# Kernel optimization log

Hardware: AMD Instinct MI355X
Metric: run time of the kernel (lower is better)

Reference implementation:

```python
import jax, jax.numpy as jnp
import numpy as np

H = 64
NG = 100000   # gene nodes
ND = 30000    # disease nodes
NE = 1500000  # gda edges (gene -> disease)
NL = 500000   # supervision (label) edges


def setup_inputs() -> dict:
    key = jax.random.key(0)
    ks = jax.random.split(key, 20)
    s = 0.1
    inp = {
        "gene_emb":    jax.random.normal(ks[0], (NG, H), jnp.float32) * s,
        "disease_emb": jax.random.normal(ks[1], (ND, H), jnp.float32) * s,
    }
    wnames = ["w1_gd_l", "w1_gd_r", "w1_dg_l", "w1_dg_r",
              "w2_gd_l", "w2_gd_r", "w2_dg_l", "w2_dg_r"]
    for i, n in enumerate(wnames):
        inp[n] = jax.random.normal(ks[2 + i], (H, H), jnp.float32) * s
    for i, n in enumerate(["b1_gd", "b1_dg", "b2_gd", "b2_dg"]):
        inp[n] = jax.random.normal(ks[10 + i], (H,), jnp.float32) * 0.01
    inp["edge_src"]  = jax.random.randint(ks[14], (NE,), 0, NG)
    inp["edge_dst"]  = jax.random.randint(ks[15], (NE,), 0, ND)
    inp["label_src"] = jax.random.randint(ks[16], (NL,), 0, NG)
    inp["label_dst"] = jax.random.randint(ks[17], (NL,), 0, ND)
    return inp


def _sage(x_src, x_dst, src, dst, n_dst, wl, wr, b):
    # SAGEConv (mean aggr): lin_l(mean_{j in N(i)} x_j) + lin_r(x_i) + b
    msum = jax.ops.segment_sum(x_src[src], dst, num_segments=n_dst)
    cnt = jax.ops.segment_sum(jnp.ones((src.shape[0], 1), x_src.dtype), dst,
                              num_segments=n_dst)
    mean = msum / jnp.maximum(cnt, 1.0)
    return mean @ wl + x_dst @ wr + b


def reference(gene_emb, disease_emb,
              w1_gd_l, w1_gd_r, b1_gd, w1_dg_l, w1_dg_r, b1_dg,
              w2_gd_l, w2_gd_r, b2_gd, w2_dg_l, w2_dg_r, b2_dg,
              edge_src, edge_dst, label_src, label_dst):
    # layer 1 (hetero: gene->disease via gda, disease->gene via rev_gda)
    h_d = jax.nn.relu(_sage(gene_emb, disease_emb, edge_src, edge_dst, ND,
                            w1_gd_l, w1_gd_r, b1_gd))
    h_g = jax.nn.relu(_sage(disease_emb, gene_emb, edge_dst, edge_src, NG,
                            w1_dg_l, w1_dg_r, b1_dg))
    # layer 2 (no activation)
    h_d2 = _sage(h_g, h_d, edge_src, edge_dst, ND, w2_gd_l, w2_gd_r, b2_gd)
    h_g2 = _sage(h_d, h_g, edge_dst, edge_src, NG, w2_dg_l, w2_dg_r, b2_dg)
    # classifier: dot product over label edges
    return jnp.sum(h_g2[label_src] * h_d2[label_dst], axis=-1)
```

## Files before the change

### kernel.cpp

```cpp
#include <hip/hip_runtime.h>
#include <hip/hip_bf16.h>

#define H 64
#define SCAN_CHUNK 512
#define NB1 512

typedef unsigned short u16;
typedef unsigned int u32;
typedef unsigned char u8;
typedef __attribute__((ext_vector_type(8))) __bf16 bf16x8;
typedef __attribute__((ext_vector_type(4))) float f32x4;
typedef __attribute__((ext_vector_type(2))) float f32x2;

__device__ __forceinline__ float bflo(u32 u) {
    return __builtin_bit_cast(float, u << 16);
}
__device__ __forceinline__ float bfhi(u32 u) {
    return __builtin_bit_cast(float, u & 0xffff0000u);
}
__device__ __forceinline__ u16 bf16rne(float f) {
    u32 u = __builtin_bit_cast(u32, f);
    return (u16)((u + 0x7FFFu + ((u >> 16) & 1u)) >> 16);
}

__global__ __launch_bounds__(256) void fused_count_convert_kernel(
    const int* __restrict__ es, const int* __restrict__ ed,
    int* __restrict__ histD, int* __restrict__ histG,
    int ne, int shiftD, int shiftG,
    const float* __restrict__ a, u16* __restrict__ oa, u32* __restrict__ oa8,
    long long na4,
    const float* __restrict__ b, u16* __restrict__ ob, long long nb4)
{
    if (blockIdx.x < NB1) {
        __shared__ int lhd[256], lhg[256];
        const int tid = threadIdx.x;
        lhd[tid] = 0; lhg[tid] = 0;
        __syncthreads();
        const int chunk = (ne + NB1 - 1) / NB1;
        const int e0 = blockIdx.x * chunk;
        const int e1 = min(e0 + chunk, ne);
        for (int e = e0 + tid; e < e1; e += 256) {
            atomicAdd(&lhd[ed[e] >> shiftD], 1);
            atomicAdd(&lhg[es[e] >> shiftG], 1);
        }
        __syncthreads();
        histD[tid * NB1 + blockIdx.x] = lhd[tid];
        histG[tid * NB1 + blockIdx.x] = lhg[tid];
        return;
    }
    long long i = (long long)(blockIdx.x - NB1) * 256 + threadIdx.x;
    if (i < na4) {
        float4 v = *(const float4*)&a[i * 4];
        ushort4 o;
        o.x = bf16rne(v.x); o.y = bf16rne(v.y);
        o.z = bf16rne(v.z); o.w = bf16rne(v.w);
        *(ushort4*)&oa[i * 4] = o;
        int r = 0;
        r = __builtin_amdgcn_cvt_pk_fp8_f32(v.x * 16.0f, v.y * 16.0f, r, false);
        r = __builtin_amdgcn_cvt_pk_fp8_f32(v.z * 16.0f, v.w * 16.0f, r, true);
        oa8[i] = (u32)r;
    } else if (i < na4 + nb4) {
        long long q = i - na4;
        float4 v = *(const float4*)&b[q * 4];
        ushort4 o;
        o.x = bf16rne(v.x); o.y = bf16rne(v.y);
        o.z = bf16rne(v.z); o.w = bf16rne(v.w);
        *(ushort4*)&ob[q * 4] = o;
    }
}

__global__ __launch_bounds__(256) void scan_reduce_kernel(
    const int* __restrict__ a1, int n1, const int* __restrict__ a2, int n2,
    int B1, int* __restrict__ partial)
{
    const int b = blockIdx.x;
    const int* a; int n, base;
    if (b < B1) { a = a1; n = n1; base = b * SCAN_CHUNK; }
    else        { a = a2; n = n2; base = (b - B1) * SCAN_CHUNK; }
    int t = threadIdx.x;
    int i0 = base + 2 * t, i1 = i0 + 1;
    int v = ((i0 < n) ? a[i0] : 0) + ((i1 < n) ? a[i1] : 0);
    #pragma unroll
    for (int off = 32; off > 0; off >>= 1) v += __shfl_down(v, off, 64);
    __shared__ int ws[4];
    if ((t & 63) == 0) ws[t >> 6] = v;
    __syncthreads();
    if (t == 0) partial[b] = ws[0] + ws[1] + ws[2] + ws[3];
}

__global__ __launch_bounds__(256) void scan_apply_kernel(
    const int* __restrict__ a1, int* __restrict__ out1, int n1,
    const int* __restrict__ a2, int* __restrict__ out2, int n2,
    int B1, int nbtot, const int* __restrict__ partial)
{
    __shared__ int sExcl[1024];
    __shared__ int ws[4];
    const int tid = threadIdx.x;
    const int lane = tid & 63, wid = tid >> 6;

    int j0 = 4 * tid;
    int p0 = (j0 + 0 < nbtot) ? partial[j0 + 0] : 0;
    int p1 = (j0 + 1 < nbtot) ? partial[j0 + 1] : 0;
    int p2 = (j0 + 2 < nbtot) ? partial[j0 + 2] : 0;
    int p3 = (j0 + 3 < nbtot) ? partial[j0 + 3] : 0;
    int psum = p0 + p1 + p2 + p3;
    int P = psum;
    #pragma unroll
    for (int off = 1; off < 64; off <<= 1) {
        int u = __shfl_up(P, off, 64);
        if (lane >= off) P += u;
    }
    if (lane == 63) ws[wid] = P;
    __syncthreads();
    int wbase = 0;
    #pragma unroll
    for (int w = 0; w < 4; ++w) wbase += (w < wid) ? ws[w] : 0;
    int e = wbase + (P - psum);
    sExcl[j0 + 0] = e;
    sExcl[j0 + 1] = e + p0;
    sExcl[j0 + 2] = e + p0 + p1;
    sExcl[j0 + 3] = e + p0 + p1 + p2;
    __syncthreads();

    const int b = blockIdx.x;
    int tot1 = sExcl[B1 - 1] + partial[B1 - 1];
    int myOff = sExcl[b] - ((b >= B1) ? tot1 : 0);
    if (b == 0 && tid == 0) {
        int tot2 = sExcl[nbtot - 1] + partial[nbtot - 1] - tot1;
        out1[n1] = tot1;
        out2[n2] = tot2;
    }
    __syncthreads();

    const int* a; int* out; int n, base;
    if (b < B1) { a = a1; out = out1; n = n1; base = b * SCAN_CHUNK; }
    else        { a = a2; out = out2; n = n2; base = (b - B1) * SCAN_CHUNK; }
    int i0 = base + 2 * tid, i1 = i0 + 1;
    int x0 = (i0 < n) ? a[i0] : 0;
    int x1 = (i1 < n) ? a[i1] : 0;
    int p = x0 + x1;
    int Q = p;
    #pragma unroll
    for (int off = 1; off < 64; off <<= 1) {
        int u = __shfl_up(Q, off, 64);
        if (lane >= off) Q += u;
    }
    if (lane == 63) ws[wid] = Q;
    __syncthreads();
    int waveBase = 0;
    #pragma unroll
    for (int w = 0; w < 4; ++w) waveBase += (w < wid) ? ws[w] : 0;
    int off0 = myOff + waveBase + (Q - p);
    if (i0 < n) out[i0] = off0;
    if (i1 < n) out[i1] = off0 + x0;
}

__global__ __launch_bounds__(256) void part_scatter_kernel(
    const int* __restrict__ es, const int* __restrict__ ed,
    const int* __restrict__ baseD, const int* __restrict__ baseG,
    u32* __restrict__ pairD, u32* __restrict__ pairG,
    int ne, int shiftD, int shiftG)
{
    __shared__ int curD[256], curG[256];
    const int tid = threadIdx.x;
    curD[tid] = baseD[tid * NB1 + blockIdx.x];
    curG[tid] = baseG[tid * NB1 + blockIdx.x];
    __syncthreads();
    const int maskD = (1 << shiftD) - 1;
    const int maskG = (1 << shiftG) - 1;
    const int chunk = (ne + NB1 - 1) / NB1;
    const int e0 = blockIdx.x * chunk;
    const int e1 = min(e0 + chunk, ne);
    for (int e = e0 + tid; e < e1; e += 256) {
        int s = es[e], d = ed[e];
        int pD = atomicAdd(&curD[d >> shiftD], 1);
        pairD[pD] = ((u32)(d & maskD) << 17) | (u32)s;
        int pG = atomicAdd(&curG[s >> shiftG], 1);
        pairG[pG] = ((u32)(s & maskG) << 17) | (u32)d;
    }
}

__global__ __launch_bounds__(256) void csr_build_kernel(
    const u32* __restrict__ pairD, const int* __restrict__ baseD,
    int* __restrict__ rowD, int* __restrict__ idxD, int nd, int shiftD, int nbktD,
    const u32* __restrict__ pairG, const int* __restrict__ baseG,
    int* __restrict__ rowG, int* __restrict__ idxG, int ng, int shiftG, int nbktG)
{
    __shared__ int lcnt[512], lcur[512];
    __shared__ int ws[4];
    const int j = blockIdx.x & 255;
    const int isG = blockIdx.x >> 8;
    const u32* pair; const int* base; int* row; int* idx; int n, shift, nbkt;
    if (isG) { pair = pairG; base = baseG; row = rowG; idx = idxG; n = ng; shift = shiftG; nbkt = nbktG; }
    else     { pair = pairD; base = baseD; row = rowD; idx = idxD; n = nd; shift = shiftD; nbkt = nbktD; }
    if (j >= nbkt) return;

    const int tid = threadIdx.x;
    const int nLo = j << shift;
    const int nHi = min(nLo + (1 << shift), n);
    const int range = nHi - nLo;
    const int segBase = base[j * NB1];
    const int segEnd  = base[(j + 1) * NB1];

    lcnt[tid] = 0; lcnt[tid + 256] = 0;
    __syncthreads();
    for (int t = segBase + tid; t < segEnd; t += 256)
        atomicAdd(&lcnt[pair[t] >> 17], 1);
    __syncthreads();

    int i0 = 2 * tid, i1 = i0 + 1;
    int c0 = (i0 < range) ? lcnt[i0] : 0;
    int c1 = (i1 < range) ? lcnt[i1] : 0;
    int p = c0 + c1;
    int P = p;
    const int lane = tid & 63, wid = tid >> 6;
    #pragma unroll
    for (int off = 1; off < 64; off <<= 1) {
        int u = __shfl_up(P, off, 64);
        if (lane >= off) P += u;
    }
    if (lane == 63) ws[wid] = P;
    __syncthreads();
    int waveBase = 0;
    #pragma unroll
    for (int w = 0; w < 4; ++w) waveBase += (w < wid) ? ws[w] : 0;
    int o0 = segBase + waveBase + (P - p);
    int o1 = o0 + c0;
    if (i0 < range) { row[nLo + i0] = o0; lcur[i0] = o0; }
    if (i1 < range) { row[nLo + i1] = o1; lcur[i1] = o1; }
    if (nHi == n && tid == 0) row[n] = segEnd;
    __syncthreads();

    for (int t = segBase + tid; t < segEnd; t += 256) {
        u32 pr = pair[t];
        int pos = atomicAdd(&lcur[pr >> 17], 1);
        idx[pos] = (int)(pr & 0x1FFFFu);
    }
}

template <bool F8D>
__global__ __launch_bounds__(256) void gather_mean_kernel(
    const void* __restrict__ srcD_, const u16* __restrict__ srcG,
    const int* __restrict__ rowD, const int* __restrict__ idxD,
    const int* __restrict__ rowG, const int* __restrict__ idxG,
    u16* __restrict__ outD, u16* __restrict__ outG, int nd, int ng)
{
    int hw = blockIdx.x * 8 + (threadIdx.x >> 5);
    int l5 = threadIdx.x & 31;
    if (hw >= nd + ng) return;
    const bool isD = hw < nd;
    const int sub = l5 >> 3;
    const int c8 = l5 & 7;
    const int* row; const int* idx; u16* out; int node;
    if (isD) { row = rowD; idx = idxD; out = outD; node = hw; }
    else     { row = rowG; idx = idxG; out = outG; node = hw - nd; }
    int beg = row[node], end = row[node + 1];

    float a0[8], a1[8];
    #pragma unroll
    for (int j = 0; j < 8; ++j) { a0[j] = 0.f; a1[j] = 0.f; }

    if (F8D && isD) {
        const u8* src8 = (const u8*)srcD_;
        int i = beg;
        for (; i + 8 <= end; i += 8) {
            int s0 = idx[i + sub];
            int s1 = idx[i + 4 + sub];
            uint2 v0 = *((const uint2*)(src8 + (size_t)s0 * 64) + c8);
            uint2 v1 = *((const uint2*)(src8 + (size_t)s1 * 64) + c8);
            f32x2 f;
            f = __builtin_amdgcn_cvt_pk_f32_fp8((int)v0.x, false); a0[0] += f.x; a0[1] += f.y;
            f = __builtin_amdgcn_cvt_pk_f32_fp8((int)v0.x, true);  a0[2] += f.x; a0[3] += f.y;
            f = __builtin_amdgcn_cvt_pk_f32_fp8((int)v0.y, false); a0[4] += f.x; a0[5] += f.y;
            f = __builtin_amdgcn_cvt_pk_f32_fp8((int)v0.y, true);  a0[6] += f.x; a0[7] += f.y;
            f = __builtin_amdgcn_cvt_pk_f32_fp8((int)v1.x, false); a1[0] += f.x; a1[1] += f.y;
            f = __builtin_amdgcn_cvt_pk_f32_fp8((int)v1.x, true);  a1[2] += f.x; a1[3] += f.y;
            f = __builtin_amdgcn_cvt_pk_f32_fp8((int)v1.y, false); a1[4] += f.x; a1[5] += f.y;
            f = __builtin_amdgcn_cvt_pk_f32_fp8((int)v1.y, true);  a1[6] += f.x; a1[7] += f.y;
        }
        if (i + 4 <= end) {
            int s0 = idx[i + sub];
            uint2 v0 = *((const uint2*)(src8 + (size_t)s0 * 64) + c8);
            f32x2 f;
            f = __builtin_amdgcn_cvt_pk_f32_fp8((int)v0.x, false); a0[0] += f.x; a0[1] += f.y;
            f = __builtin_amdgcn_cvt_pk_f32_fp8((int)v0.x, true);  a0[2] += f.x; a0[3] += f.y;
            f = __builtin_amdgcn_cvt_pk_f32_fp8((int)v0.y, false); a0[4] += f.x; a0[5] += f.y;
            f = __builtin_amdgcn_cvt_pk_f32_fp8((int)v0.y, true);  a0[6] += f.x; a0[7] += f.y;
            i += 4;
        }
        if (i + sub < end) {
            int s1 = idx[i + sub];
            uint2 v1 = *((const uint2*)(src8 + (size_t)s1 * 64) + c8);
            f32x2 f;
            f = __builtin_amdgcn_cvt_pk_f32_fp8((int)v1.x, false); a1[0] += f.x; a1[1] += f.y;
            f = __builtin_amdgcn_cvt_pk_f32_fp8((int)v1.x, true);  a1[2] += f.x; a1[3] += f.y;
            f = __builtin_amdgcn_cvt_pk_f32_fp8((int)v1.y, false); a1[4] += f.x; a1[5] += f.y;
            f = __builtin_amdgcn_cvt_pk_f32_fp8((int)v1.y, true);  a1[6] += f.x; a1[7] += f.y;
        }
    } else {
        const u16* src = isD ? (const u16*)srcD_ : srcG;
        int i = beg;
        for (; i + 8 <= end; i += 8) {
            int s0 = idx[i + sub];
            int s1 = idx[i + 4 + sub];
            uint4 v0 = *((const uint4*)(src + (size_t)s0 * H) + c8);
            uint4 v1 = *((const uint4*)(src + (size_t)s1 * H) + c8);
            a0[0] += bflo(v0.x); a0[1] += bfhi(v0.x); a0[2] += bflo(v0.y); a0[3] += bfhi(v0.y);
            a0[4] += bflo(v0.z); a0[5] += bfhi(v0.z); a0[6] += bflo(v0.w); a0[7] += bfhi(v0.w);
            a1[0] += bflo(v1.x); a1[1] += bfhi(v1.x); a1[2] += bflo(v1.y); a1[3] += bfhi(v1.y);
            a1[4] += bflo(v1.z); a1[5] += bfhi(v1.z); a1[6] += bflo(v1.w); a1[7] += bfhi(v1.w);
        }
        if (i + 4 <= end) {
            int s0 = idx[i + sub];
            uint4 v0 = *((const uint4*)(src + (size_t)s0 * H) + c8);
            a0[0] += bflo(v0.x); a0[1] += bfhi(v0.x); a0[2] += bflo(v0.y); a0[3] += bfhi(v0.y);
            a0[4] += bflo(v0.z); a0[5] += bfhi(v0.z); a0[6] += bflo(v0.w); a0[7] += bfhi(v0.w);
            i += 4;
        }
        if (i + sub < end) {
            int s1 = idx[i + sub];
            uint4 v1 = *((const uint4*)(src + (size_t)s1 * H) + c8);
            a1[0] += bflo(v1.x); a1[1] += bfhi(v1.x); a1[2] += bflo(v1.y); a1[3] += bfhi(v1.y);
            a1[4] += bflo(v1.z); a1[5] += bfhi(v1.z); a1[6] += bflo(v1.w); a1[7] += bfhi(v1.w);
        }
    }

    float acc[8];
    #pragma unroll
    for (int j = 0; j < 8; ++j) acc[j] = a0[j] + a1[j];
    #pragma unroll
    for (int j = 0; j < 8; ++j) {
        acc[j] += __shfl_xor(acc[j], 8, 64);
        acc[j] += __shfl_xor(acc[j], 16, 64);
    }
    if (sub == 0) {
        float inv = 1.0f / fmaxf((float)(end - beg), 1.0f);
        if (F8D && isD) inv *= 0.0625f;
        u32 w0 = (u32)bf16rne(acc[0] * inv) | ((u32)bf16rne(acc[1] * inv) << 16);
        u32 w1 = (u32)bf16rne(acc[2] * inv) | ((u32)bf16rne(acc[3] * inv) << 16);
        u32 w2 = (u32)bf16rne(acc[4] * inv) | ((u32)bf16rne(acc[5] * inv) << 16);
        u32 w3 = (u32)bf16rne(acc[6] * inv) | ((u32)bf16rne(acc[7] * inv) << 16);
        uint4 pk = make_uint4(w0, w1, w2, w3);
        *(uint4*)(out + (size_t)node * H + c8 * 8) = pk;
    }
}

template <bool RELU>
__global__ __launch_bounds__(256) void sage_mm_mfma_kernel(
    const u16* __restrict__ meanD, const u16* __restrict__ xD, u16* __restrict__ outD,
    const float* __restrict__ wlD, const float* __restrict__ wrD,
    const float* __restrict__ bD, int nd,
    const u16* __restrict__ meanG, const u16* __restrict__ xG, u16* __restrict__ outG,
    const float* __restrict__ wlG, const float* __restrict__ wrG,
    const float* __restrict__ bG, int ng, int MBD)
{
    __shared__ u16 sB[16 * 64 * 8];
    int b = blockIdx.x;
    const u16 *mean, *x; u16* out; const float *wl, *wr, *bias; int n;
    if (b < MBD) { mean = meanD; x = xD; out = outD; wl = wlD; wr = wrD; bias = bD; n = nd; }
    else { b -= MBD; mean = meanG; x = xG; out = outG; wl = wlG; wr = wrG; bias = bG; n = ng; }

    const int tid = threadIdx.x;
    for (int i = tid; i < 4096; i += 256) {
        int k = i >> 6, ncol = i & 63;
        int q = (k >> 3) & 3, j = k & 7, t = ncol >> 4, n15 = ncol & 15;
        int lane = q * 16 + n15;
        int c0 = k >> 5;
        sB[(((c0 + 0) * 4 + t) * 64 + lane) * 8 + j] = bf16rne(wl[i]);
        sB[(((c0 + 2) * 4 + t) * 64 + lane) * 8 + j] = bf16rne(wr[i]);
    }
    __syncthreads();

    const int lane = tid & 63;
    const int wave = tid >> 6;
    const int m = lane & 15;
    const int q = lane >> 4;

    bf16x8 Bf[16];
    {
        const uint4* sB4 = (const uint4*)sB;
        #pragma unroll
        for (int f = 0; f < 16; ++f)
            Bf[f] = __builtin_bit_cast(bf16x8, sB4[f * 64 + lane]);
    }
    float bv[4];
    #pragma unroll
    for (int t = 0; t < 4; ++t) bv[t] = bias[t * 16 + m];

    const int row0 = b * 256;
    #pragma unroll
    for (int r = 0; r < 4; ++r) {
        int rbase = row0 + (wave + 4 * r) * 16;
        if (rbase >= n) break;
        int gr = min(rbase + m, n - 1);
        const uint4* mrow = (const uint4*)(mean + (size_t)gr * H);
        const uint4* xrow = (const uint4*)(x + (size_t)gr * H);
        bf16x8 A0 = __builtin_bit_cast(bf16x8, mrow[q]);
        bf16x8 A1 = __builtin_bit_cast(bf16x8, mrow[q + 4]);
        bf16x8 A2 = __builtin_bit_cast(bf16x8, xrow[q]);
        bf16x8 A3 = __builtin_bit_cast(bf16x8, xrow[q + 4]);
        f32x4 acc[4];
        #pragma unroll
        for (int t = 0; t < 4; ++t) acc[t] = (f32x4){bv[t], bv[t], bv[t], bv[t]};
        #pragma unroll
        for (int t = 0; t < 4; ++t) {
            acc[t] = __builtin_amdgcn_mfma_f32_16x16x32_bf16(A0, Bf[0 * 4 + t], acc[t], 0, 0, 0);
            acc[t] = __builtin_amdgcn_mfma_f32_16x16x32_bf16(A1, Bf[1 * 4 + t], acc[t], 0, 0, 0);
            acc[t] = __builtin_amdgcn_mfma_f32_16x16x32_bf16(A2, Bf[2 * 4 + t], acc[t], 0, 0, 0);
            acc[t] = __builtin_amdgcn_mfma_f32_16x16x32_bf16(A3, Bf[3 * 4 + t], acc[t], 0, 0, 0);
        }
        #pragma unroll
        for (int reg = 0; reg < 4; ++reg) {
            int orow = rbase + q * 4 + reg;
            if (orow < n) {
                u16* op = out + (size_t)orow * H;
                #pragma unroll
                for (int t = 0; t < 4; ++t) {
                    float v = acc[t][reg];
                    if (RELU) v = fmaxf(v, 0.0f);
                    op[t * 16 + m] = bf16rne(v);
                }
            }
        }
    }
}

__global__ __launch_bounds__(256) void classify_kernel(
    const u16* __restrict__ hg2, const u16* __restrict__ hd2,
    const int* __restrict__ ls, const int* __restrict__ ld,
    float* __restrict__ out, int nl)
{
    long long t = (long long)blockIdx.x * blockDim.x + threadIdx.x;
    int e = (int)(t >> 3);
    int c8 = (int)(t & 7);
    if (e >= nl) return;
    int a = ls[e];
    int b = ld[e];
    uint4 ua = *((const uint4*)(hg2 + (size_t)a * H) + c8);
    uint4 ub = *((const uint4*)(hd2 + (size_t)b * H) + c8);
    float v = bflo(ua.x) * bflo(ub.x) + bfhi(ua.x) * bfhi(ub.x)
            + bflo(ua.y) * bflo(ub.y) + bfhi(ua.y) * bfhi(ub.y)
            + bflo(ua.z) * bflo(ub.z) + bfhi(ua.z) * bfhi(ub.z)
            + bflo(ua.w) * bflo(ub.w) + bfhi(ua.w) * bfhi(ub.w);
    v += __shfl_xor(v, 1, 64);
    v += __shfl_xor(v, 2, 64);
    v += __shfl_xor(v, 4, 64);
    if (c8 == 0) out[e] = v;
}

extern "C" void kernel_launch(void* const* d_in, const int* in_sizes, int n_in,
                              void* d_out, int out_size, void* d_ws, size_t ws_size,
                              hipStream_t stream)
{
    const float* gene  = (const float*)d_in[0];
    const float* dis   = (const float*)d_in[1];
    const float* w1gdl = (const float*)d_in[2];
    const float* w1gdr = (const float*)d_in[3];
    const float* w1dgl = (const float*)d_in[4];
    const float* w1dgr = (const float*)d_in[5];
    const float* w2gdl = (const float*)d_in[6];
    const float* w2gdr = (const float*)d_in[7];
    const float* w2dgl = (const float*)d_in[8];
    const float* w2dgr = (const float*)d_in[9];
    const float* b1gd  = (const float*)d_in[10];
    const float* b1dg  = (const float*)d_in[11];
    const float* b2gd  = (const float*)d_in[12];
    const float* b2dg  = (const float*)d_in[13];
    const int* es = (const int*)d_in[14];
    const int* ed = (const int*)d_in[15];
    const int* ls = (const int*)d_in[16];
    const int* ld = (const int*)d_in[17];

    const int ng = in_sizes[0] / H;
    const int nd = in_sizes[1] / H;
    const int ne = in_sizes[14];
    const int nl = in_sizes[16];

    int shiftD = 0; while (((nd + (1 << shiftD) - 1) >> shiftD) > 256) ++shiftD;
    int shiftG = 0; while (((ng + (1 << shiftG) - 1) >> shiftG) > 256) ++shiftG;
    const int nbktD = (nd + (1 << shiftD) - 1) >> shiftD;
    const int nbktG = (ng + (1 << shiftG) - 1) >> shiftG;
    const int n1 = 256 * NB1;

    int* rowD = (int*)d_ws;
    int* rowG = rowD + nd + 1;
    int* idxD = rowG + ng + 1;
    int* idxG = idxD + ne;
    u16* geneBf = (u16*)(idxG + ne);
    u16* disBf  = geneBf + (size_t)ng * H;
    u16* h1Dbf  = disBf + (size_t)nd * H;
    u16* h1Gbf  = h1Dbf + (size_t)nd * H;
    u16* h2Dbf  = h1Gbf + (size_t)ng * H;
    u16* h2Gbf  = h2Dbf + (size_t)nd * H;
    uintptr_t pf8 = (uintptr_t)(h2Gbf + (size_t)ng * H);
    pf8 = (pf8 + 15) & ~(uintptr_t)15;
    u32* geneF8 = (u32*)pf8;
    uintptr_t p = (uintptr_t)(geneF8 + (size_t)ng * 16);
    p = (p + 15) & ~(uintptr_t)15;
    u16* MD = (u16*)p;
    u16* MG = MD + (size_t)nd * H;
    int* histD = (int*)p;
    int* histG = histD + n1;
    int* baseD = histG + n1;
    int* baseG = baseD + n1 + 1;
    int* partial  = baseG + n1 + 1;
    uintptr_t pp = (uintptr_t)(partial + 1024);
    pp = (pp + 15) & ~(uintptr_t)15;
    u32* pairD = (u32*)pp;
    u32* pairG = pairD + ne;

    const long long na4 = (long long)ng * H / 4;
    const long long nb4 = (long long)nd * H / 4;
    const int convBlocks = (int)((na4 + nb4 + 255) / 256);
    fused_count_convert_kernel<<<NB1 + convBlocks, 256, 0, stream>>>(
        es, ed, histD, histG, ne, shiftD, shiftG,
        gene, geneBf, geneF8, na4, dis, disBf, nb4);

    const int B1 = n1 / SCAN_CHUNK;
    const int nbtot = 2 * B1;
    scan_reduce_kernel<<<nbtot, 256, 0, stream>>>(histD, n1, histG, n1, B1, partial);
    scan_apply_kernel<<<nbtot, 256, 0, stream>>>(histD, baseD, n1,
                                                 histG, baseG, n1, B1, nbtot, partial);

    part_scatter_kernel<<<NB1, 256, 0, stream>>>(es, ed, baseD, baseG,
                                                 pairD, pairG, ne, shiftD, shiftG);
    csr_build_kernel<<<512, 256, 0, stream>>>(
        pairD, baseD, rowD, idxD, nd, shiftD, nbktD,
        pairG, baseG, rowG, idxG, ng, shiftG, nbktG);

    const int gatherBlocks = (nd + ng + 7) / 8;
    const int MBD = (nd + 255) / 256;
    const int MBG = (ng + 255) / 256;

    gather_mean_kernel<true><<<gatherBlocks, 256, 0, stream>>>(
        geneF8, disBf, rowD, idxD, rowG, idxG, MD, MG, nd, ng);
    sage_mm_mfma_kernel<true><<<MBD + MBG, 256, 0, stream>>>(
        MD, disBf, h1Dbf, w1gdl, w1gdr, b1gd, nd,
        MG, geneBf, h1Gbf, w1dgl, w1dgr, b1dg, ng, MBD);

    gather_mean_kernel<false><<<gatherBlocks, 256, 0, stream>>>(
        h1Gbf, h1Dbf, rowD, idxD, rowG, idxG, MD, MG, nd, ng);
    sage_mm_mfma_kernel<false><<<MBD + MBG, 256, 0, stream>>>(
        MD, h1Dbf, h2Dbf, w2gdl, w2gdr, b2gd, nd,
        MG, h1Gbf, h2Gbf, w2dgl, w2dgr, b2dg, ng, MBD);

    {
        long long threads = (long long)nl * 8;
        int blocks = (int)((threads + 255) / 256);
        classify_kernel<<<blocks, 256, 0, stream>>>(h2Gbf, h2Dbf, ls, ld,
                                                    (float*)d_out, nl);
    }
}
```

Measured before the change: 349.8 us.

## Fuse neighbor mean gather into MFMA SAGE matmul and bucket-sort label edges

Merges the gather-mean kernel and the MFMA linear kernel into one 512-thread kernel. Each block gathers 128 rows of neighbor means into shared memory and then multiplies them, so the mean buffers no longer make a round trip through global memory and two launches per layer are dropped. It also adds a bucket partition of label edges by source gene, reusing the histogram, scan and scatter stages, so the classifier reads gene rows in near-sorted order for better cache locality. The cost is more shared memory per block, heavier per-block work, and extra preprocessing passes over the label edges.

```diff
diff --git a/kernel.cpp b/kernel.cpp
--- a/kernel.cpp
+++ b/kernel.cpp
@@ -4,6 +4,9 @@
 #define H 64
 #define SCAN_CHUNK 512
 #define NB1 512
+#define NBL 256
+#define MROWS 128
+#define MSTRIDE 72
 
 typedef unsigned short u16;
 typedef unsigned int u32;
@@ -27,6 +30,7 @@
     const int* __restrict__ es, const int* __restrict__ ed,
     int* __restrict__ histD, int* __restrict__ histG,
     int ne, int shiftD, int shiftG,
+    const int* __restrict__ ls, int* __restrict__ histL, int nl,
     const float* __restrict__ a, u16* __restrict__ oa, u32* __restrict__ oa8,
     long long na4,
     const float* __restrict__ b, u16* __restrict__ ob, long long nb4)
@@ -48,7 +52,22 @@
         histG[tid * NB1 + blockIdx.x] = lhg[tid];
         return;
     }
-    long long i = (long long)(blockIdx.x - NB1) * 256 + threadIdx.x;
+    if (blockIdx.x < NB1 + NBL) {
+        __shared__ int lhl[256];
+        const int tid = threadIdx.x;
+        const int blk = blockIdx.x - NB1;
+        lhl[tid] = 0;
+        __syncthreads();
+        const int chunk = (nl + NBL - 1) / NBL;
+        const int e0 = blk * chunk;
+        const int e1 = min(e0 + chunk, nl);
+        for (int e = e0 + tid; e < e1; e += 256)
+            atomicAdd(&lhl[ls[e] >> shiftG], 1);
+        __syncthreads();
+        histL[tid * NBL + blk] = lhl[tid];
+        return;
+    }
+    long long i = (long long)(blockIdx.x - NB1 - NBL) * 256 + threadIdx.x;
     if (i < na4) {
         float4 v = *(const float4*)&a[i * 4];
         ushort4 o;
@@ -70,13 +89,15 @@
 }
 
 __global__ __launch_bounds__(256) void scan_reduce_kernel(
-    const int* __restrict__ a1, int n1, const int* __restrict__ a2, int n2,
-    int B1, int* __restrict__ partial)
+    const int* __restrict__ a1, int n1_, const int* __restrict__ a2, int n2_,
+    const int* __restrict__ a3, int n3_, int B1, int B2,
+    int* __restrict__ partial)
 {
     const int b = blockIdx.x;
     const int* a; int n, base;
-    if (b < B1) { a = a1; n = n1; base = b * SCAN_CHUNK; }
-    else        { a = a2; n = n2; base = (b - B1) * SCAN_CHUNK; }
+    if (b < B1)          { a = a1; n = n1_; base = b * SCAN_CHUNK; }
+    else if (b < B1 + B2){ a = a2; n = n2_; base = (b - B1) * SCAN_CHUNK; }
+    else                 { a = a3; n = n3_; base = (b - B1 - B2) * SCAN_CHUNK; }
     int t = threadIdx.x;
     int i0 = base + 2 * t, i1 = i0 + 1;
     int v = ((i0 < n) ? a[i0] : 0) + ((i1 < n) ? a[i1] : 0);
@@ -89,9 +110,10 @@
 }
 
 __global__ __launch_bounds__(256) void scan_apply_kernel(
-    const int* __restrict__ a1, int* __restrict__ out1, int n1,
-    const int* __restrict__ a2, int* __restrict__ out2, int n2,
-    int B1, int nbtot, const int* __restrict__ partial)
+    const int* __restrict__ a1, int* __restrict__ out1, int n1_,
+    const int* __restrict__ a2, int* __restrict__ out2, int n2_,
+    const int* __restrict__ a3, int* __restrict__ out3, int n3_,
+    int B1, int B2, int nbtot, const int* __restrict__ partial)
 {
     __shared__ int sExcl[1024];
     __shared__ int ws[4];
@@ -124,17 +146,21 @@
 
     const int b = blockIdx.x;
     int tot1 = sExcl[B1 - 1] + partial[B1 - 1];
-    int myOff = sExcl[b] - ((b >= B1) ? tot1 : 0);
+    int totA = sExcl[B1 + B2 - 1] + partial[B1 + B2 - 1];
+    int tot2 = totA - tot1;
+    int myOff = sExcl[b] - ((b >= B1) ? tot1 : 0) - ((b >= B1 + B2) ? tot2 : 0);
     if (b == 0 && tid == 0) {
-        int tot2 = sExcl[nbtot - 1] + partial[nbtot - 1] - tot1;
-        out1[n1] = tot1;
-        out2[n2] = tot2;
+        int tot3 = sExcl[nbtot - 1] + partial[nbtot - 1] - totA;
+        out1[n1_] = tot1;
+        out2[n2_] = tot2;
+        out3[n3_] = tot3;
     }
     __syncthreads();
 
     const int* a; int* out; int n, base;
-    if (b < B1) { a = a1; out = out1; n = n1; base = b * SCAN_CHUNK; }
-    else        { a = a2; out = out2; n = n2; base = (b - B1) * SCAN_CHUNK; }
+    if (b < B1)          { a = a1; out = out1; n = n1_; base = b * SCAN_CHUNK; }
+    else if (b < B1 + B2){ a = a2; out = out2; n = n2_; base = (b - B1) * SCAN_CHUNK; }
+    else                 { a = a3; out = out3; n = n3_; base = (b - B1 - B2) * SCAN_CHUNK; }
     int i0 = base + 2 * tid, i1 = i0 + 1;
     int x0 = (i0 < n) ? a[i0] : 0;
     int x1 = (i1 < n) ? a[i1] : 0;
@@ -159,24 +185,39 @@
     const int* __restrict__ es, const int* __restrict__ ed,
     const int* __restrict__ baseD, const int* __restrict__ baseG,
     u32* __restrict__ pairD, u32* __restrict__ pairG,
-    int ne, int shiftD, int shiftG)
-{
-    __shared__ int curD[256], curG[256];
+    int ne, int shiftD, int shiftG,
+    const int* __restrict__ ls, const int* __restrict__ baseL,
+    int* __restrict__ permL, int nl)
+{
+    __shared__ int curA[256], curB[256];
     const int tid = threadIdx.x;
-    curD[tid] = baseD[tid * NB1 + blockIdx.x];
-    curG[tid] = baseG[tid * NB1 + blockIdx.x];
-    __syncthreads();
-    const int maskD = (1 << shiftD) - 1;
-    const int maskG = (1 << shiftG) - 1;
-    const int chunk = (ne + NB1 - 1) / NB1;
-    const int e0 = blockIdx.x * chunk;
-    const int e1 = min(e0 + chunk, ne);
-    for (int e = e0 + tid; e < e1; e += 256) {
-        int s = es[e], d = ed[e];
-        int pD = atomicAdd(&curD[d >> shiftD], 1);
-        pairD[pD] = ((u32)(d & maskD) << 17) | (u32)s;
-        int pG = atomicAdd(&curG[s >> shiftG], 1);
-        pairG[pG] = ((u32)(s & maskG) << 17) | (u32)d;
+    if (blockIdx.x < NB1) {
+        curA[tid] = baseD[tid * NB1 + blockIdx.x];
+        curB[tid] = baseG[tid * NB1 + blockIdx.x];
+        __syncthreads();
+        const int maskD = (1 << shiftD) - 1;
+        const int maskG = (1 << shiftG) - 1;
+        const int chunk = (ne + NB1 - 1) / NB1;
+        const int e0 = blockIdx.x * chunk;
+        const int e1 = min(e0 + chunk, ne);
+        for (int e = e0 + tid; e < e1; e += 256) {
+            int s = es[e], d = ed[e];
+            int pD = atomicAdd(&curA[d >> shiftD], 1);
+            pairD[pD] = ((u32)(d & maskD) << 17) | (u32)s;
+            int pG = atomicAdd(&curB[s >> shiftG], 1);
+            pairG[pG] = ((u32)(s & maskG) << 17) | (u32)d;
+        }
+    } else {
+        const int blk = blockIdx.x - NB1;
+        curA[tid] = baseL[tid * NBL + blk];
+        __syncthreads();
+        const int chunk = (nl + NBL - 1) / NBL;
+        const int e0 = blk * chunk;
+        const int e1 = min(e0 + chunk, nl);
+        for (int e = e0 + tid; e < e1; e += 256) {
+            int pos = atomicAdd(&curA[ls[e] >> shiftG], 1);
+            permL[pos] = e;
+        }
     }
 }
 
@@ -238,130 +279,37 @@
     }
 }
 
-template <bool F8D>
-__global__ __launch_bounds__(256) void gather_mean_kernel(
-    const void* __restrict__ srcD_, const u16* __restrict__ srcG,
+template <bool RELU, bool F8D>
+__global__ __launch_bounds__(512, 8) void fused_gather_mm_kernel(
+    const void* __restrict__ gsrcD, const u16* __restrict__ gsrcG,
     const int* __restrict__ rowD, const int* __restrict__ idxD,
     const int* __restrict__ rowG, const int* __restrict__ idxG,
-    u16* __restrict__ outD, u16* __restrict__ outG, int nd, int ng)
-{
-    int hw = blockIdx.x * 8 + (threadIdx.x >> 5);
-    int l5 = threadIdx.x & 31;
-    if (hw >= nd + ng) return;
-    const bool isD = hw < nd;
-    const int sub = l5 >> 3;
-    const int c8 = l5 & 7;
-    const int* row; const int* idx; u16* out; int node;
-    if (isD) { row = rowD; idx = idxD; out = outD; node = hw; }
-    else     { row = rowG; idx = idxG; out = outG; node = hw - nd; }
-    int beg = row[node], end = row[node + 1];
-
-    float a0[8], a1[8];
-    #pragma unroll
-    for (int j = 0; j < 8; ++j) { a0[j] = 0.f; a1[j] = 0.f; }
-
-    if (F8D && isD) {
-        const u8* src8 = (const u8*)srcD_;
-        int i = beg;
-        for (; i + 8 <= end; i += 8) {
-            int s0 = idx[i + sub];
-            int s1 = idx[i + 4 + sub];
-            uint2 v0 = *((const uint2*)(src8 + (size_t)s0 * 64) + c8);
-            uint2 v1 = *((const uint2*)(src8 + (size_t)s1 * 64) + c8);
-            f32x2 f;
-            f = __builtin_amdgcn_cvt_pk_f32_fp8((int)v0.x, false); a0[0] += f.x; a0[1] += f.y;
-            f = __builtin_amdgcn_cvt_pk_f32_fp8((int)v0.x, true);  a0[2] += f.x; a0[3] += f.y;
-            f = __builtin_amdgcn_cvt_pk_f32_fp8((int)v0.y, false); a0[4] += f.x; a0[5] += f.y;
-            f = __builtin_amdgcn_cvt_pk_f32_fp8((int)v0.y, true);  a0[6] += f.x; a0[7] += f.y;
-            f = __builtin_amdgcn_cvt_pk_f32_fp8((int)v1.x, false); a1[0] += f.x; a1[1] += f.y;
-            f = __builtin_amdgcn_cvt_pk_f32_fp8((int)v1.x, true);  a1[2] += f.x; a1[3] += f.y;
-            f = __builtin_amdgcn_cvt_pk_f32_fp8((int)v1.y, false); a1[4] += f.x; a1[5] += f.y;
-            f = __builtin_amdgcn_cvt_pk_f32_fp8((int)v1.y, true);  a1[6] += f.x; a1[7] += f.y;
-        }
-        if (i + 4 <= end) {
-            int s0 = idx[i + sub];
-            uint2 v0 = *((const uint2*)(src8 + (size_t)s0 * 64) + c8);
-            f32x2 f;
-            f = __builtin_amdgcn_cvt_pk_f32_fp8((int)v0.x, false); a0[0] += f.x; a0[1] += f.y;
-            f = __builtin_amdgcn_cvt_pk_f32_fp8((int)v0.x, true);  a0[2] += f.x; a0[3] += f.y;
-            f = __builtin_amdgcn_cvt_pk_f32_fp8((int)v0.y, false); a0[4] += f.x; a0[5] += f.y;
-            f = __builtin_amdgcn_cvt_pk_f32_fp8((int)v0.y, true);  a0[6] += f.x; a0[7] += f.y;
-            i += 4;
-        }
-        if (i + sub < end) {
-            int s1 = idx[i + sub];
-            uint2 v1 = *((const uint2*)(src8 + (size_t)s1 * 64) + c8);
-            f32x2 f;
-            f = __builtin_amdgcn_cvt_pk_f32_fp8((int)v1.x, false); a1[0] += f.x; a1[1] += f.y;
-            f = __builtin_amdgcn_cvt_pk_f32_fp8((int)v1.x, true);  a1[2] += f.x; a1[3] += f.y;
-            f = __builtin_amdgcn_cvt_pk_f32_fp8((int)v1.y, false); a1[4] += f.x; a1[5] += f.y;
-            f = __builtin_amdgcn_cvt_pk_f32_fp8((int)v1.y, true);  a1[6] += f.x; a1[7] += f.y;
-        }
+    const u16* __restrict__ xD, const u16* __restrict__ xG,
+    u16* __restrict__ outD, u16* __restrict__ outG,
+    const float* __restrict__ wlD, const float* __restrict__ wrD,
+    const float* __restrict__ bD,
+    const float* __restrict__ wlG, const float* __restrict__ wrG,
+    const float* __restrict__ bG,
+    int nd, int ng, int MBD)
+{
+    __shared__ u16 sB[16 * 64 * 8];
+    __shared__ u16 sM[MROWS * MSTRIDE];
+
+    int b = blockIdx.x;
+    const void* gsrc; const int* row; const int* idx; const u16* x; u16* out;
+    const float *wl, *wr, *bias; int n; bool isD;
+    if (b < MBD) {
+        isD = true;  gsrc = gsrcD; row = rowD; idx = idxD; x = xD; out = outD;
+        wl = wlD; wr = wrD; bias = bD; n = nd;
     } else {
-        const u16* src = isD ? (const u16*)srcD_ : srcG;
-        int i = beg;
-        for (; i + 8 <= end; i += 8) {
-            int s0 = idx[i + sub];
-            int s1 = idx[i + 4 + sub];
-            uint4 v0 = *((const uint4*)(src + (size_t)s0 * H) + c8);
-            uint4 v1 = *((const uint4*)(src + (size_t)s1 * H) + c8);
-            a0[0] += bflo(v0.x); a0[1] += bfhi(v0.x); a0[2] += bflo(v0.y); a0[3] += bfhi(v0.y);
-            a0[4] += bflo(v0.z); a0[5] += bfhi(v0.z); a0[6] += bflo(v0.w); a0[7] += bfhi(v0.w);
-            a1[0] += bflo(v1.x); a1[1] += bfhi(v1.x); a1[2] += bflo(v1.y); a1[3] += bfhi(v1.y);
-            a1[4] += bflo(v1.z); a1[5] += bfhi(v1.z); a1[6] += bflo(v1.w); a1[7] += bfhi(v1.w);
-        }
-        if (i + 4 <= end) {
-            int s0 = idx[i + sub];
-            uint4 v0 = *((const uint4*)(src + (size_t)s0 * H) + c8);
-            a0[0] += bflo(v0.x); a0[1] += bfhi(v0.x); a0[2] += bflo(v0.y); a0[3] += bfhi(v0.y);
-            a0[4] += bflo(v0.z); a0[5] += bfhi(v0.z); a0[6] += bflo(v0.w); a0[7] += bfhi(v0.w);
-            i += 4;
-        }
-        if (i + sub < end) {
-            int s1 = idx[i + sub];
-            uint4 v1 = *((const uint4*)(src + (size_t)s1 * H) + c8);
-            a1[0] += bflo(v1.x); a1[1] += bfhi(v1.x); a1[2] += bflo(v1.y); a1[3] += bfhi(v1.y);
-            a1[4] += bflo(v1.z); a1[5] += bfhi(v1.z); a1[6] += bflo(v1.w); a1[7] += bfhi(v1.w);
-        }
-    }
-
-    float acc[8];
-    #pragma unroll
-    for (int j = 0; j < 8; ++j) acc[j] = a0[j] + a1[j];
-    #pragma unroll
-    for (int j = 0; j < 8; ++j) {
-        acc[j] += __shfl_xor(acc[j], 8, 64);
-        acc[j] += __shfl_xor(acc[j], 16, 64);
-    }
-    if (sub == 0) {
-        float inv = 1.0f / fmaxf((float)(end - beg), 1.0f);
-        if (F8D && isD) inv *= 0.0625f;
-        u32 w0 = (u32)bf16rne(acc[0] * inv) | ((u32)bf16rne(acc[1] * inv) << 16);
-        u32 w1 = (u32)bf16rne(acc[2] * inv) | ((u32)bf16rne(acc[3] * inv) << 16);
-        u32 w2 = (u32)bf16rne(acc[4] * inv) | ((u32)bf16rne(acc[5] * inv) << 16);
-        u32 w3 = (u32)bf16rne(acc[6] * inv) | ((u32)bf16rne(acc[7] * inv) << 16);
-        uint4 pk = make_uint4(w0, w1, w2, w3);
-        *(uint4*)(out + (size_t)node * H + c8 * 8) = pk;
-    }
-}
-
-template <bool RELU>
-__global__ __launch_bounds__(256) void sage_mm_mfma_kernel(
-    const u16* __restrict__ meanD, const u16* __restrict__ xD, u16* __restrict__ outD,
-    const float* __restrict__ wlD, const float* __restrict__ wrD,
-    const float* __restrict__ bD, int nd,
-    const u16* __restrict__ meanG, const u16* __restrict__ xG, u16* __restrict__ outG,
-    const float* __restrict__ wlG, const float* __restrict__ wrG,
-    const float* __restrict__ bG, int ng, int MBD)
-{
-    __shared__ u16 sB[16 * 64 * 8];
-    int b = blockIdx.x;
-    const u16 *mean, *x; u16* out; const float *wl, *wr, *bias; int n;
-    if (b < MBD) { mean = meanD; x = xD; out = outD; wl = wlD; wr = wrD; bias = bD; n = nd; }
-    else { b -= MBD; mean = meanG; x = xG; out = outG; wl = wlG; wr = wrG; bias = bG; n = ng; }
-
+        b -= MBD;
+        isD = false; gsrc = (const void*)gsrcG; row = rowG; idx = idxG; x = xG;
+        out = outG; wl = wlG; wr = wrG; bias = bG; n = ng;
+    }
+    const int row0 = b * MROWS;
     const int tid = threadIdx.x;
-    for (int i = tid; i < 4096; i += 256) {
+
+    for (int i = tid; i < 4096; i += 512) {
         int k = i >> 6, ncol = i & 63;
         int q = (k >> 3) & 3, j = k & 7, t = ncol >> 4, n15 = ncol & 15;
         int lane = q * 16 + n15;
@@ -369,57 +317,150 @@
         sB[(((c0 + 0) * 4 + t) * 64 + lane) * 8 + j] = bf16rne(wl[i]);
         sB[(((c0 + 2) * 4 + t) * 64 + lane) * 8 + j] = bf16rne(wr[i]);
     }
+
+    {
+        const int hw = tid >> 5;
+        const int l5 = tid & 31;
+        const int sub = l5 >> 3;
+        const int c8 = l5 & 7;
+        for (int t = 0; t < 8; ++t) {
+            int lr = hw * 8 + t;
+            int node = row0 + lr;
+            if (node >= n) break;
+            int beg = row[node], end = row[node + 1];
+            float a0[8], a1[8];
+            #pragma unroll
+            for (int j = 0; j < 8; ++j) { a0[j] = 0.f; a1[j] = 0.f; }
+
+            if (F8D && isD) {
+                const u8* src8 = (const u8*)gsrc;
+                int i = beg;
+                for (; i + 8 <= end; i += 8) {
+                    int s0 = idx[i + sub];
+                    int s1 = idx[i + 4 + sub];
+                    uint2 v0 = *((const uint2*)(src8 + (size_t)s0 * 64) + c8);
+                    uint2 v1 = *((const uint2*)(src8 + (size_t)s1 * 64) + c8);
+                    f32x2 f;
+                    f = __builtin_amdgcn_cvt_pk_f32_fp8((int)v0.x, false); a0[0] += f.x; a0[1] += f.y;
+                    f = __builtin_amdgcn_cvt_pk_f32_fp8((int)v0.x, true);  a0[2] += f.x; a0[3] += f.y;
+                    f = __builtin_amdgcn_cvt_pk_f32_fp8((int)v0.y, false); a0[4] += f.x; a0[5] += f.y;
+                    f = __builtin_amdgcn_cvt_pk_f32_fp8((int)v0.y, true);  a0[6] += f.x; a0[7] += f.y;
+                    f = __builtin_amdgcn_cvt_pk_f32_fp8((int)v1.x, false); a1[0] += f.x; a1[1] += f.y;
+                    f = __builtin_amdgcn_cvt_pk_f32_fp8((int)v1.x, true);  a1[2] += f.x; a1[3] += f.y;
+                    f = __builtin_amdgcn_cvt_pk_f32_fp8((int)v1.y, false); a1[4] += f.x; a1[5] += f.y;
+                    f = __builtin_amdgcn_cvt_pk_f32_fp8((int)v1.y, true);  a1[6] += f.x; a1[7] += f.y;
+                }
+                if (i + 4 <= end) {
+                    int s0 = idx[i + sub];
+                    uint2 v0 = *((const uint2*)(src8 + (size_t)s0 * 64) + c8);
+                    f32x2 f;
+                    f = __builtin_amdgcn_cvt_pk_f32_fp8((int)v0.x, false); a0[0] += f.x; a0[1] += f.y;
+                    f = __builtin_amdgcn_cvt_pk_f32_fp8((int)v0.x, true);  a0[2] += f.x; a0[3] += f.y;
+                    f = __builtin_amdgcn_cvt_pk_f32_fp8((int)v0.y, false); a0[4] += f.x; a0[5] += f.y;
+                    f = __builtin_amdgcn_cvt_pk_f32_fp8((int)v0.y, true);  a0[6] += f.x; a0[7] += f.y;
+                    i += 4;
+                }
+                if (i + sub < end) {
+                    int s1 = idx[i + sub];
+                    uint2 v1 = *((const uint2*)(src8 + (size_t)s1 * 64) + c8);
+                    f32x2 f;
+                    f = __builtin_amdgcn_cvt_pk_f32_fp8((int)v1.x, false); a1[0] += f.x; a1[1] += f.y;
+                    f = __builtin_amdgcn_cvt_pk_f32_fp8((int)v1.x, true);  a1[2] += f.x; a1[3] += f.y;
+                    f = __builtin_amdgcn_cvt_pk_f32_fp8((int)v1.y, false); a1[4] += f.x; a1[5] += f.y;
+                    f = __builtin_amdgcn_cvt_pk_f32_fp8((int)v1.y, true);  a1[6] += f.x; a1[7] += f.y;
+                }
+            } else {
+                const u16* src = (const u16*)gsrc;
+                int i = beg;
+                for (; i + 8 <= end; i += 8) {
+                    int s0 = idx[i + sub];
+                    int s1 = idx[i + 4 + sub];
+                    uint4 v0 = *((const uint4*)(src + (size_t)s0 * H) + c8);
+                    uint4 v1 = *((const uint4*)(src + (size_t)s1 * H) + c8);
+                    a0[0] += bflo(v0.x); a0[1] += bfhi(v0.x); a0[2] += bflo(v0.y); a0[3] += bfhi(v0.y);
+                    a0[4] += bflo(v0.z); a0[5] += bfhi(v0.z); a0[6] += bflo(v0.w); a0[7] += bfhi(v0.w);
+                    a1[0] += bflo(v1.x); a1[1] += bfhi(v1.x); a1[2] += bflo(v1.y); a1[3] += bfhi(v1.y);
+                    a1[4] += bflo(v1.z); a1[5] += bfhi(v1.z); a1[6] += bflo(v1.w); a1[7] += bfhi(v1.w);
+                }
+                if (i + 4 <= end) {
+                    int s0 = idx[i + sub];
+                    uint4 v0 = *((const uint4*)(src + (size_t)s0 * H) + c8);
+                    a0[0] += bflo(v0.x); a0[1] += bfhi(v0.x); a0[2] += bflo(v0.y); a0[3] += bfhi(v0.y);
+                    a0[4] += bflo(v0.z); a0[5] += bfhi(v0.z); a0[6] += bflo(v0.w); a0[7] += bfhi(v0.w);
+                    i += 4;
+                }
+                if (i + sub < end) {
+                    int s1 = idx[i + sub];
+                    uint4 v1 = *((const uint4*)(src + (size_t)s1 * H) + c8);
+                    a1[0] += bflo(v1.x); a1[1] += bfhi(v1.x); a1[2] += bflo(v1.y); a1[3] += bfhi(v1.y);
+                    a1[4] += bflo(v1.z); a1[5] += bfhi(v1.z); a1[6] += bflo(v1.w); a1[7] += bfhi(v1.w);
+                }
+            }
+
+            float acc[8];
+            #pragma unroll
+            for (int j = 0; j < 8; ++j) acc[j] = a0[j] + a1[j];
+            #pragma unroll
+            for (int j = 0; j < 8; ++j) {
+                acc[j] += __shfl_xor(acc[j], 8, 64);
+                acc[j] += __shfl_xor(acc[j], 16, 64);
+            }
+            if (sub == 0) {
+                float inv = 1.0f / fmaxf((float)(end - beg), 1.0f);
+                if (F8D && isD) inv *= 0.0625f;
+                u32 w0 = (u32)bf16rne(acc[0] * inv) | ((u32)bf16rne(acc[1] * inv) << 16);
+                u32 w1 = (u32)bf16rne(acc[2] * inv) | ((u32)bf16rne(acc[3] * inv) << 16);
+                u32 w2 = (u32)bf16rne(acc[4] * inv) | ((u32)bf16rne(acc[5] * inv) << 16);
+                u32 w3 = (u32)bf16rne(acc[6] * inv) | ((u32)bf16rne(acc[7] * inv) << 16);
+                *(uint4*)(sM + lr * MSTRIDE + c8 * 8) = make_uint4(w0, w1, w2, w3);
+            }
+        }
+    }
     __syncthreads();
 
     const int lane = tid & 63;
     const int wave = tid >> 6;
     const int m = lane & 15;
     const int q = lane >> 4;
-
-    bf16x8 Bf[16];
-    {
-        const uint4* sB4 = (const uint4*)sB;
-        #pragma unroll
-        for (int f = 0; f < 16; ++f)
-            Bf[f] = __builtin_bit_cast(bf16x8, sB4[f * 64 + lane]);
-    }
-    float bv[4];
-    #pragma unroll
-    for (int t = 0; t < 4; ++t) bv[t] = bias[t * 16 + m];
-
-    const int row0 = b * 256;
-    #pragma unroll
-    for (int r = 0; r < 4; ++r) {
-        int rbase = row0 + (wave + 4 * r) * 16;
-        if (rbase >= n) break;
-        int gr = min(rbase + m, n - 1);
-        const uint4* mrow = (const uint4*)(mean + (size_t)gr * H);
-        const uint4* xrow = (const uint4*)(x + (size_t)gr * H);
-        bf16x8 A0 = __builtin_bit_cast(bf16x8, mrow[q]);
-        bf16x8 A1 = __builtin_bit_cast(bf16x8, mrow[q + 4]);
-        bf16x8 A2 = __builtin_bit_cast(bf16x8, xrow[q]);
-        bf16x8 A3 = __builtin_bit_cast(bf16x8, xrow[q + 4]);
-        f32x4 acc[4];
-        #pragma unroll
-        for (int t = 0; t < 4; ++t) acc[t] = (f32x4){bv[t], bv[t], bv[t], bv[t]};
-        #pragma unroll
-        for (int t = 0; t < 4; ++t) {
-            acc[t] = __builtin_amdgcn_mfma_f32_16x16x32_bf16(A0, Bf[0 * 4 + t], acc[t], 0, 0, 0);
-            acc[t] = __builtin_amdgcn_mfma_f32_16x16x32_bf16(A1, Bf[1 * 4 + t], acc[t], 0, 0, 0);
-            acc[t] = __builtin_amdgcn_mfma_f32_16x16x32_bf16(A2, Bf[2 * 4 + t], acc[t], 0, 0, 0);
-            acc[t] = __builtin_amdgcn_mfma_f32_16x16x32_bf16(A3, Bf[3 * 4 + t], acc[t], 0, 0, 0);
-        }
-        #pragma unroll
-        for (int reg = 0; reg < 4; ++reg) {
-            int orow = rbase + q * 4 + reg;
-            if (orow < n) {
-                u16* op = out + (size_t)orow * H;
-                #pragma unroll
-                for (int t = 0; t < 4; ++t) {
-                    float v = acc[t][reg];
-                    if (RELU) v = fmaxf(v, 0.0f);
-                    op[t * 16 + m] = bf16rne(v);
-                }
+    int rbase = row0 + wave * 16;
+    if (rbase >= n) return;
+
+    const u16* mrowp = sM + (wave * 16 + m) * MSTRIDE;
+    bf16x8 A0 = __builtin_bit_cast(bf16x8, *(const uint4*)(mrowp + q * 8));
+    bf16x8 A1 = __builtin_bit_cast(bf16x8, *(const uint4*)(mrowp + q * 8 + 32));
+    int gr = min(rbase + m, n - 1);
+    const uint4* xrow = (const uint4*)(x + (size_t)gr * H);
+    bf16x8 A2 = __builtin_bit_cast(bf16x8, xrow[q]);
+    bf16x8 A3 = __builtin_bit_cast(bf16x8, xrow[q + 4]);
+
+    f32x4 acc[4];
+    #pragma unroll
+    for (int t = 0; t < 4; ++t) {
+        float bv = bias[t * 16 + m];
+        acc[t] = (f32x4){bv, bv, bv, bv};
+    }
+    const uint4* sB4 = (const uint4*)sB;
+    #pragma unroll
+    for (int t = 0; t < 4; ++t) {
+        bf16x8 B0 = __builtin_bit_cast(bf16x8, sB4[(0 * 4 + t) * 64 + lane]);
+        acc[t] = __builtin_amdgcn_mfma_f32_16x16x32_bf16(A0, B0, acc[t], 0, 0, 0);
+        bf16x8 B1 = __builtin_bit_cast(bf16x8, sB4[(1 * 4 + t) * 64 + lane]);
+        acc[t] = __builtin_amdgcn_mfma_f32_16x16x32_bf16(A1, B1, acc[t], 0, 0, 0);
+        bf16x8 B2 = __builtin_bit_cast(bf16x8, sB4[(2 * 4 + t) * 64 + lane]);
+        acc[t] = __builtin_amdgcn_mfma_f32_16x16x32_bf16(A2, B2, acc[t], 0, 0, 0);
+        bf16x8 B3 = __builtin_bit_cast(bf16x8, sB4[(3 * 4 + t) * 64 + lane]);
+        acc[t] = __builtin_amdgcn_mfma_f32_16x16x32_bf16(A3, B3, acc[t], 0, 0, 0);
+    }
+    #pragma unroll
+    for (int reg = 0; reg < 4; ++reg) {
+        int orow = rbase + q * 4 + reg;
+        if (orow < n) {
+            u16* op = out + (size_t)orow * H;
+            #pragma unroll
+            for (int t = 0; t < 4; ++t) {
+                float v = acc[t][reg];
+                if (RELU) v = fmaxf(v, 0.0f);
+                op[t * 16 + m] = bf16rne(v);
             }
         }
     }
@@ -428,12 +469,14 @@
 __global__ __launch_bounds__(256) void classify_kernel(
     const u16* __restrict__ hg2, const u16* __restrict__ hd2,
     const int* __restrict__ ls, const int* __restrict__ ld,
+    const int* __restrict__ permL,
     float* __restrict__ out, int nl)
 {
     long long t = (long long)blockIdx.x * blockDim.x + threadIdx.x;
-    int e = (int)(t >> 3);
+    int i = (int)(t >> 3);
     int c8 = (int)(t & 7);
-    if (e >= nl) return;
+    if (i >= nl) return;
+    int e = permL[i];
     int a = ls[e];
     int b = ld[e];
     uint4 ua = *((const uint4*)(hg2 + (size_t)a * H) + c8);
@@ -481,12 +524,14 @@
     const int nbktD = (nd + (1 << shiftD) - 1) >> shiftD;
     const int nbktG = (ng + (1 << shiftG) - 1) >> shiftG;
     const int n1 = 256 * NB1;
+    const int n3 = 256 * NBL;
 
     int* rowD = (int*)d_ws;
     int* rowG = rowD + nd + 1;
     int* idxD = rowG + ng + 1;
     int* idxG = idxD + ne;
-    u16* geneBf = (u16*)(idxG + ne);
+    int* permL = idxG + ne;
+    u16* geneBf = (u16*)(permL + nl);
     u16* disBf  = geneBf + (size_t)ng * H;
     u16* h1Dbf  = disBf + (size_t)nd * H;
     u16* h1Gbf  = h1Dbf + (size_t)nd * H;
@@ -497,13 +542,13 @@
     u32* geneF8 = (u32*)pf8;
     uintptr_t p = (uintptr_t)(geneF8 + (size_t)ng * 16);
     p = (p + 15) & ~(uintptr_t)15;
-    u16* MD = (u16*)p;
-    u16* MG = MD + (size_t)nd * H;
     int* histD = (int*)p;
     int* histG = histD + n1;
-    int* baseD = histG + n1;
+    int* histL = histG + n1;
+    int* baseD = histL + n3;
     int* baseG = baseD + n1 + 1;
-    int* partial  = baseG + n1 + 1;
+    int* baseL = baseG + n1 + 1;
+    int* partial = baseL + n3 + 1;
     uintptr_t pp = (uintptr_t)(partial + 1024);
     pp = (pp + 15) & ~(uintptr_t)15;
     u32* pairD = (u32*)pp;
@@ -512,42 +557,47 @@
     const long long na4 = (long long)ng * H / 4;
     const long long nb4 = (long long)nd * H / 4;
     const int convBlocks = (int)((na4 + nb4 + 255) / 256);
-    fused_count_convert_kernel<<<NB1 + convBlocks, 256, 0, stream>>>(
+    fused_count_convert_kernel<<<NB1 + NBL + convBlocks, 256, 0, stream>>>(
         es, ed, histD, histG, ne, shiftD, shiftG,
+        ls, histL, nl,
         gene, geneBf, geneF8, na4, dis, disBf, nb4);
 
     const int B1 = n1 / SCAN_CHUNK;
-    const int nbtot = 2 * B1;
-    scan_reduce_kernel<<<nbtot, 256, 0, stream>>>(histD, n1, histG, n1, B1, partial);
+    const int B2 = B1;
+    const int B3 = n3 / SCAN_CHUNK;
+    const int nbtot = B1 + B2 + B3;
+    scan_reduce_kernel<<<nbtot, 256, 0, stream>>>(histD, n1, histG, n1,
+                                                  histL, n3, B1, B2, partial);
     scan_apply_kernel<<<nbtot, 256, 0, stream>>>(histD, baseD, n1,
-                                                 histG, baseG, n1, B1, nbtot, partial);
-
-    part_scatter_kernel<<<NB1, 256, 0, stream>>>(es, ed, baseD, baseG,
-                                                 pairD, pairG, ne, shiftD, shiftG);
+                                                 histG, baseG, n1,
+                                                 histL, baseL, n3,
+                                                 B1, B2, nbtot, partial);
+
+    part_scatter_kernel<<<NB1 + NBL, 256, 0, stream>>>(
+        es, ed, baseD, baseG, pairD, pairG, ne, shiftD, shiftG,
+        ls, baseL, permL, nl);
+
     csr_build_kernel<<<512, 256, 0, stream>>>(
         pairD, baseD, rowD, idxD, nd, shiftD, nbktD,
         pairG, baseG, rowG, idxG, ng, shiftG, nbktG);
 
-    const int gatherBlocks = (nd + ng + 7) / 8;
-    const int MBD = (nd + 255) / 256;
-    const int MBG = (ng + 255) / 256;
-
-    gather_mean_kernel<true><<<gatherBlocks, 256, 0, stream>>>(
-        geneF8, disBf, rowD, idxD, rowG, idxG, MD, MG, nd, ng);
-    sage_mm_mfma_kernel<true><<<MBD + MBG, 256, 0, stream>>>(
-        MD, disBf, h1Dbf, w1gdl, w1gdr, b1gd, nd,
-        MG, geneBf, h1Gbf, w1dgl, w1dgr, b1dg, ng, MBD);
-
-    gather_mean_kernel<false><<<gatherBlocks, 256, 0, stream>>>(
-        h1Gbf, h1Dbf, rowD, idxD, rowG, idxG, MD, MG, nd, ng);
-    sage_mm_mfma_kernel<false><<<MBD + MBG, 256, 0, stream>>>(
-        MD, h1Dbf, h2Dbf, w2gdl, w2gdr, b2gd, nd,
-        MG, h1Gbf, h2Gbf, w2dgl, w2dgr, b2dg, ng, MBD);
+    const int MBD = (nd + MROWS - 1) / MROWS;
+    const int MBG = (ng + MROWS - 1) / MROWS;
+
+    fused_gather_mm_kernel<true, true><<<MBD + MBG, 512, 0, stream>>>(
+        geneF8, disBf, rowD, idxD, rowG, idxG,
+        disBf, geneBf, h1Dbf, h1Gbf,
+        w1gdl, w1gdr, b1gd, w1dgl, w1dgr, b1dg, nd, ng, MBD);
+
+    fused_gather_mm_kernel<false, false><<<MBD + MBG, 512, 0, stream>>>(
+        h1Gbf, h1Dbf, rowD, idxD, rowG, idxG,
+        h1Dbf, h1Gbf, h2Dbf, h2Gbf,
+        w2gdl, w2gdr, b2gd, w2dgl, w2dgr, b2dg, nd, ng, MBD);
 
     {
         long long threads = (long long)nl * 8;
         int blocks = (int)((threads + 255) / 256);
         classify_kernel<<<blocks, 256, 0, stream>>>(h2Gbf, h2Dbf, ls, ld,
-                                                    (float*)d_out, nl);
-    }
-}
+                                                    permL, (float*)d_out, nl);
+    }
+}
```

New measurement: 377.4 us. 7.9% more time.
